# Kernel optimization log

Measured on AMD Instinct MI355X. Metric: run time of the kernel, lower is better.

## Reference

```python
import jax, jax.numpy as jnp
import numpy as np

EPS = 1e-6
POOL = (2, 2)
STRIDE = (2, 2)


def setup_inputs() -> dict:
    key = jax.random.key(0)
    k1, k2, k3 = jax.random.split(key, 3)
    B, H, W, C = 32, 256, 256, 128
    x = jax.random.normal(k1, (B, H, W, C), dtype=jnp.float32)
    entropy_weights = jax.random.normal(k2, (C,), dtype=jnp.float32)
    pooling_bias = jax.random.normal(k3, (C,), dtype=jnp.float32)
    return {"x": x, "entropy_weights": entropy_weights, "pooling_bias": pooling_bias}


def reference(x, entropy_weights, pooling_bias):
    # NHWC input; pool_size == strides == (2,2): non-overlapping windows.
    B, H, W, C = x.shape
    ph, pw = POOL
    Ho = (H - ph) // STRIDE[0] + 1
    Wo = (W - pw) // STRIDE[1] + 1
    # [B, Ho, ph, Wo, pw, C] -> [B, Ho, Wo, ph*pw, C]
    windows = x.reshape(B, Ho, ph, Wo, pw, C).transpose(0, 1, 3, 2, 4, 5)
    windows = windows.reshape(B, Ho, Wo, ph * pw, C)
    # per-window softmax across the ph*pw elements (per channel)
    p = jax.nn.softmax(windows, axis=3)
    # entropy reduction over window elements
    entropy = -jnp.sum(p * jnp.log(p + EPS), axis=3)  # [B, Ho, Wo, C]
    # learnable per-channel affine
    return entropy * entropy_weights + pooling_bias
```

## Files before the change

kernel.cpp:

```cpp
#include <hip/hip_runtime.h>
#include <hip/hip_bf16.h>


#define B_  32
#define H_  256
#define W_  256
#define C_  128

__global__ __launch_bounds__(256) void entropy_pool_kernel(
    const float4* __restrict__ x,
    const float*  __restrict__ w,
    const float*  __restrict__ bias,
    float4* __restrict__ out)
{
    const unsigned t  = blockIdx.x * blockDim.x + threadIdx.x;
    const unsigned c4 = t & 31u;
    unsigned tmp      = t >> 5;
    const unsigned wo = tmp & 127u;
    tmp >>= 7;
    const unsigned ho = tmp & 127u;
    const unsigned b  = tmp >> 7;

    const unsigned base = ((b * H_ + 2u * ho) * W_ + 2u * wo) * (C_ / 4) + c4;
    const float4 v00 = x[base];
    const float4 v01 = x[base + (C_ / 4)];
    const float4 v10 = x[base + W_ * (C_ / 4)];
    const float4 v11 = x[base + W_ * (C_ / 4) + (C_ / 4)];

    const float4 wv = ((const float4*)w)[c4];
    const float4 bv = ((const float4*)bias)[c4];

    float4 r;
    #pragma unroll
    for (int j = 0; j < 4; ++j) {
        float a0, a1, a2, a3, wj, bj;
        switch (j) {
            case 0: a0=v00.x; a1=v01.x; a2=v10.x; a3=v11.x; wj=wv.x; bj=bv.x; break;
            case 1: a0=v00.y; a1=v01.y; a2=v10.y; a3=v11.y; wj=wv.y; bj=bv.y; break;
            case 2: a0=v00.z; a1=v01.z; a2=v10.z; a3=v11.z; wj=wv.z; bj=bv.z; break;
            default:a0=v00.w; a1=v01.w; a2=v10.w; a3=v11.w; wj=wv.w; bj=bv.w; break;
        }
        const float m  = fmaxf(fmaxf(a0, a1), fmaxf(a2, a3));
        const float d0 = a0 - m, d1 = a1 - m, d2 = a2 - m, d3 = a3 - m;
        const float e0 = __expf(d0), e1 = __expf(d1), e2 = __expf(d2), e3 = __expf(d3);
        const float s  = e0 + e1 + e2 + e3;
        const float ws = e0 * d0 + e1 * d1 + e2 * d2 + e3 * d3;
        const float entropy = __logf(s) - ws * __frcp_rn(s);
        const float o = entropy * wj + bj;
        switch (j) {
            case 0: r.x = o; break;
            case 1: r.y = o; break;
            case 2: r.z = o; break;
            default:r.w = o; break;
        }
    }
    out[t] = r;
}

extern "C" void kernel_launch(void* const* d_in, const int* in_sizes, int n_in,
                              void* d_out, int out_size, void* d_ws, size_t ws_size,
                              hipStream_t stream) {
    const float4* x   = (const float4*)d_in[0];
    const float*  w   = (const float*)d_in[1];
    const float*  bia = (const float*)d_in[2];
    float4* out       = (float4*)d_out;

    const int threads = 256;
    const int total4  = out_size / 4;
    const int blocks  = total4 / threads;
    entropy_pool_kernel<<<blocks, threads, 0, stream>>>(x, w, bia, out);
}
```

Measured before the change: 1.392 ms.

## Use grid-stride loop, two windows per thread, and nontemporal loads/stores

Each thread now handles two adjacent pooling windows, issuing eight 16-byte loads before any compute, which raises memory-level parallelism. The launch becomes a fixed 2048-block grid-stride loop, and loads and stores use nontemporal hints to avoid polluting cache with streaming data. The kernel is memory bound, so any gain depends on better bandwidth utilisation; the fixed grid and higher register use could lower occupancy.

```diff
diff --git a/kernel.cpp b/kernel.cpp
--- a/kernel.cpp
+++ b/kernel.cpp
@@ -1,72 +1,83 @@
 #include <hip/hip_runtime.h>
-#include <hip/hip_bf16.h>
 
 
 #define B_  32
 #define H_  256
 #define W_  256
 #define C_  128
+#define HO_ 128
+#define WO_ 128
+
+#define TOTAL_WI (B_ * HO_ * (WO_ / 2) * (C_ / 4))
+
+typedef float f32x4 __attribute__((ext_vector_type(4)));
+
+__device__ __forceinline__ float entropy1(float a0, float a1, float a2, float a3) {
+    const float m  = fmaxf(fmaxf(a0, a1), fmaxf(a2, a3));
+    const float d0 = a0 - m, d1 = a1 - m, d2 = a2 - m, d3 = a3 - m;
+    const float e0 = __expf(d0), e1 = __expf(d1), e2 = __expf(d2), e3 = __expf(d3);
+    const float s  = e0 + e1 + e2 + e3;
+    const float ws = e0 * d0 + e1 * d1 + e2 * d2 + e3 * d3;
+    return __logf(s) - ws * __frcp_rn(s);
+}
+
+__device__ __forceinline__ f32x4 win_entropy(f32x4 v00, f32x4 v01, f32x4 v10, f32x4 v11,
+                                             f32x4 wv, f32x4 bv) {
+    f32x4 r;
+    r.x = entropy1(v00.x, v01.x, v10.x, v11.x) * wv.x + bv.x;
+    r.y = entropy1(v00.y, v01.y, v10.y, v11.y) * wv.y + bv.y;
+    r.z = entropy1(v00.z, v01.z, v10.z, v11.z) * wv.z + bv.z;
+    r.w = entropy1(v00.w, v01.w, v10.w, v11.w) * wv.w + bv.w;
+    return r;
+}
 
 __global__ __launch_bounds__(256) void entropy_pool_kernel(
-    const float4* __restrict__ x,
-    const float*  __restrict__ w,
-    const float*  __restrict__ bias,
-    float4* __restrict__ out)
+    const f32x4* __restrict__ x,
+    const float* __restrict__ w,
+    const float* __restrict__ bias,
+    f32x4* __restrict__ out)
 {
-    const unsigned t  = blockIdx.x * blockDim.x + threadIdx.x;
-    const unsigned c4 = t & 31u;
-    unsigned tmp      = t >> 5;
-    const unsigned wo = tmp & 127u;
-    tmp >>= 7;
-    const unsigned ho = tmp & 127u;
-    const unsigned b  = tmp >> 7;
+    const unsigned tid0   = blockIdx.x * blockDim.x + threadIdx.x;
+    const unsigned stride = gridDim.x * blockDim.x;
+    const unsigned c4     = tid0 & 31u;
 
-    const unsigned base = ((b * H_ + 2u * ho) * W_ + 2u * wo) * (C_ / 4) + c4;
-    const float4 v00 = x[base];
-    const float4 v01 = x[base + (C_ / 4)];
-    const float4 v10 = x[base + W_ * (C_ / 4)];
-    const float4 v11 = x[base + W_ * (C_ / 4) + (C_ / 4)];
+    const f32x4 wv = ((const f32x4*)w)[c4];
+    const f32x4 bv = ((const f32x4*)bias)[c4];
 
-    const float4 wv = ((const float4*)w)[c4];
-    const float4 bv = ((const float4*)bias)[c4];
+    for (unsigned t = tid0; t < (unsigned)TOTAL_WI; t += stride) {
+        const unsigned wo2 = (t >> 5) & 63u;
+        const unsigned ho  = (t >> 11) & 127u;
+        const unsigned b   = t >> 18;
 
-    float4 r;
-    #pragma unroll
-    for (int j = 0; j < 4; ++j) {
-        float a0, a1, a2, a3, wj, bj;
-        switch (j) {
-            case 0: a0=v00.x; a1=v01.x; a2=v10.x; a3=v11.x; wj=wv.x; bj=bv.x; break;
-            case 1: a0=v00.y; a1=v01.y; a2=v10.y; a3=v11.y; wj=wv.y; bj=bv.y; break;
-            case 2: a0=v00.z; a1=v01.z; a2=v10.z; a3=v11.z; wj=wv.z; bj=bv.z; break;
-            default:a0=v00.w; a1=v01.w; a2=v10.w; a3=v11.w; wj=wv.w; bj=bv.w; break;
-        }
-        const float m  = fmaxf(fmaxf(a0, a1), fmaxf(a2, a3));
-        const float d0 = a0 - m, d1 = a1 - m, d2 = a2 - m, d3 = a3 - m;
-        const float e0 = __expf(d0), e1 = __expf(d1), e2 = __expf(d2), e3 = __expf(d3);
-        const float s  = e0 + e1 + e2 + e3;
-        const float ws = e0 * d0 + e1 * d1 + e2 * d2 + e3 * d3;
-        const float entropy = __logf(s) - ws * __frcp_rn(s);
-        const float o = entropy * wj + bj;
-        switch (j) {
-            case 0: r.x = o; break;
-            case 1: r.y = o; break;
-            case 2: r.z = o; break;
-            default:r.w = o; break;
-        }
+        const unsigned base = ((b * H_ + 2u * ho) * W_ + 4u * wo2) * (C_ / 4) + c4;
+
+        const f32x4 p0 = __builtin_nontemporal_load(&x[base]);
+        const f32x4 p1 = __builtin_nontemporal_load(&x[base + 32]);
+        const f32x4 p2 = __builtin_nontemporal_load(&x[base + 64]);
+        const f32x4 p3 = __builtin_nontemporal_load(&x[base + 96]);
+        const f32x4 q0 = __builtin_nontemporal_load(&x[base + 8192]);
+        const f32x4 q1 = __builtin_nontemporal_load(&x[base + 8192 + 32]);
+        const f32x4 q2 = __builtin_nontemporal_load(&x[base + 8192 + 64]);
+        const f32x4 q3 = __builtin_nontemporal_load(&x[base + 8192 + 96]);
+
+        const f32x4 rA = win_entropy(p0, p1, q0, q1, wv, bv);
+        const f32x4 rB = win_entropy(p2, p3, q2, q3, wv, bv);
+
+        const unsigned obase = ((b * HO_ + ho) * WO_ + 2u * wo2) * (C_ / 4) + c4;
+        __builtin_nontemporal_store(rA, &out[obase]);
+        __builtin_nontemporal_store(rB, &out[obase + 32]);
     }
-    out[t] = r;
 }
 
 extern "C" void kernel_launch(void* const* d_in, const int* in_sizes, int n_in,
                               void* d_out, int out_size, void* d_ws, size_t ws_size,
                               hipStream_t stream) {
-    const float4* x   = (const float4*)d_in[0];
-    const float*  w   = (const float*)d_in[1];
-    const float*  bia = (const float*)d_in[2];
-    float4* out       = (float4*)d_out;
+    const f32x4* x   = (const f32x4*)d_in[0];
+    const float* w   = (const float*)d_in[1];
+    const float* bia = (const float*)d_in[2];
+    f32x4* out       = (f32x4*)d_out;
 
     const int threads = 256;
-    const int total4  = out_size / 4;
-    const int blocks  = total4 / threads;
+    const int blocks  = 2048;
     entropy_pool_kernel<<<blocks, threads, 0, stream>>>(x, w, bia, out);
 }
```

After: 1.384 ms. About the same (-0.6%).
